# Performance work log

Measured on AMD Instinct MI355X. Metric: run time of the kernel, lower is better.

Reference implementation:

```python
import jax, jax.numpy as jnp
import numpy as np

D_MODEL = 2048
N_HEADS = 16
N_KV_HEADS = 4
HEAD_DIM = 128
ROPE_THETA = 1000000.0
B, T = 2, 2048


def setup_inputs() -> dict:
    key = jax.random.key(0)
    ks = jax.random.split(key, 5)
    s_in = 1.0 / np.sqrt(D_MODEL)
    s_o = 1.0 / np.sqrt(N_HEADS * HEAD_DIM)
    return {
        "x": jax.random.normal(ks[0], (B, T, D_MODEL), jnp.float32),
        "w_q": jax.random.normal(ks[1], (N_HEADS * HEAD_DIM, D_MODEL), jnp.float32) * s_in,
        "w_k": jax.random.normal(ks[2], (N_KV_HEADS * HEAD_DIM, D_MODEL), jnp.float32) * s_in,
        "w_v": jax.random.normal(ks[3], (N_KV_HEADS * HEAD_DIM, D_MODEL), jnp.float32) * s_in,
        "w_o": jax.random.normal(ks[4], (D_MODEL, N_HEADS * HEAD_DIM), jnp.float32) * s_o,
    }


def _rope_cos_sin(T, dtype):
    # inv_freq over even dims, emb = concat(freqs, freqs) (HF/llama convention)
    inv_freq = 1.0 / (ROPE_THETA ** (jnp.arange(0, HEAD_DIM, 2, dtype=jnp.float32) / HEAD_DIM))
    freqs = jnp.arange(T, dtype=jnp.float32)[:, None] * inv_freq[None, :]  # [T, hd/2]
    emb = jnp.concatenate([freqs, freqs], axis=-1)  # [T, hd]
    return jnp.cos(emb).astype(dtype), jnp.sin(emb).astype(dtype)


def _rotate_half(x):
    x1, x2 = jnp.split(x, 2, axis=-1)
    return jnp.concatenate([-x2, x1], axis=-1)


def reference(x, w_q, w_k, w_v, w_o):
    B, T, D = x.shape
    # QKV projections (bias=False), split heads -> [B, H, T, hd]
    q = (x @ w_q.T).reshape(B, T, N_HEADS, HEAD_DIM).transpose(0, 2, 1, 3)
    k = (x @ w_k.T).reshape(B, T, N_KV_HEADS, HEAD_DIM).transpose(0, 2, 1, 3)
    v = (x @ w_v.T).reshape(B, T, N_KV_HEADS, HEAD_DIM).transpose(0, 2, 1, 3)
    # RoPE
    cos, sin = _rope_cos_sin(T, x.dtype)  # [T, hd]
    q = q * cos + _rotate_half(q) * sin
    k = k * cos + _rotate_half(k) * sin
    # GQA: expand kv heads (repeat_interleave over head dim)
    rep = N_HEADS // N_KV_HEADS
    k = jnp.repeat(k, rep, axis=1)
    v = jnp.repeat(v, rep, axis=1)
    # Eager attention: QK^T * scale + causal mask, softmax, PV
    scale = HEAD_DIM ** -0.5
    scores = jnp.einsum("bhtd,bhsd->bhts", q, k) * scale
    causal = jnp.tril(jnp.ones((T, T), dtype=bool))
    scores = jnp.where(causal[None, None], scores, jnp.finfo(scores.dtype).min)
    probs = jax.nn.softmax(scores, axis=-1)
    out = jnp.einsum("bhts,bhsd->bhtd", probs, v)  # [B, H, T, hd]
    out = out.transpose(0, 2, 1, 3).reshape(B, T, N_HEADS * HEAD_DIM)
    return out @ w_o.T
```

## Files before the change

### kernel.cpp

```cpp
#include <hip/hip_runtime.h>
#include <cstdint>
#include <cstddef>

typedef unsigned short u16;
typedef unsigned u32;
typedef unsigned long long u64;
typedef __attribute__((ext_vector_type(8))) short short8;
typedef __attribute__((ext_vector_type(4))) float f32x4;

#define T_SEQ 2048
#define DM    2048
#define NHEAD 16
#define NKV   4
#define HD    128
#define NEGBIG (-3.0e38f)
#define QSCALE 0.1275525165017459f
#define L2IF (-0.31143258583318043f)

__device__ __forceinline__ u16 f2bf(float f) {
  union { float f; unsigned u; } c; c.f = f;
  return (u16)((c.u + 0x7fffu + ((c.u >> 16) & 1u)) >> 16);
}
__device__ __forceinline__ float bf2f(u16 b) {
  union { float f; unsigned u; } c; c.u = ((unsigned)b) << 16;
  return c.f;
}
__device__ __forceinline__ void gl_lds16(const u16* g, u16* l) {
  __builtin_amdgcn_global_load_lds(
      (const __attribute__((address_space(1))) void*)g,
      (__attribute__((address_space(3))) void*)l, 16, 0, 0);
}

#define FENCE() asm volatile("" ::: "memory")
#define BAR() do { FENCE(); __builtin_amdgcn_s_barrier(); FENCE(); } while (0)
#define WAITV4() asm volatile("s_waitcnt vmcnt(4)" ::: "memory")
#define WAITV3() asm volatile("s_waitcnt vmcnt(3)" ::: "memory")
#define WAITV0() asm volatile("s_waitcnt vmcnt(0)" ::: "memory")

__global__ void castk_all(const float* __restrict__ x, const float* __restrict__ wq,
                          const float* __restrict__ wk, const float* __restrict__ wv,
                          const float* __restrict__ wo, u16* __restrict__ dst) {
  long long i4 = (long long)blockIdx.x * 256 + threadIdx.x;
  const float* src; long long off;
  if (i4 < (2LL << 20))                    { src = x;  off = i4; }
  else if (i4 < (3LL << 20))               { src = wq; off = i4 - (2LL << 20); }
  else if (i4 < (3LL << 20) + (1 << 18))   { src = wk; off = i4 - (3LL << 20); }
  else if (i4 < (3LL << 20) + (2 << 18))   { src = wv; off = i4 - (3LL << 20) - (1 << 18); }
  else                                     { src = wo; off = i4 - (3LL << 20) - (2 << 18); }
  float4 v = *(const float4*)(src + off * 4);
  u16* d = dst + i4 * 4;
  d[0] = f2bf(v.x); d[1] = f2bf(v.y); d[2] = f2bf(v.z); d[3] = f2bf(v.w);
}

__global__ void tabk(float2* __restrict__ Tab) {
  int idx = blockIdx.x * 256 + threadIdx.x;
  float ang = (float)(idx >> 6) * exp2f((float)(idx & 63) * L2IF);
  float sn, cs;
  sincosf(ang, &sn, &cs);
  Tab[idx] = make_float2(cs, sn);
}

__global__ void ropek(u16* __restrict__ buf, const float2* __restrict__ Tab) {
  int idx = blockIdx.x * 256 + threadIdx.x;
  int r = idx >> 6, i = idx & 63;
  int t = r & (T_SEQ - 1);
  float2 cs = Tab[(t << 6) + i];
  size_t base = (size_t)r * HD + i;
  float x1 = bf2f(buf[base]), x2 = bf2f(buf[base + 64]);
  buf[base]      = f2bf(x1 * cs.x - x2 * cs.y);
  buf[base + 64] = f2bf(x2 * cs.x + x1 * cs.y);
}


template <int FH>
__device__ __forceinline__ void mfma_quad(f32x4 (&acc)[8][4], const short8 (&af)[4],
                                          const short8 (&bfr)[4]) {
#pragma unroll
  for (int i = 0; i < 4; ++i)
#pragma unroll
    for (int j = 0; j < 4; ++j)
      acc[FH * 4 + i][j] =
          __builtin_amdgcn_mfma_f32_16x16x32_bf16(af[i], bfr[j], acc[FH * 4 + i][j], 0, 0, 0);
}

template <int MODE>
__global__ __launch_bounds__(512, 2) void gemm8(
    const u16* __restrict__ A, const u16* __restrict__ Bm,
    void* __restrict__ Out0, u16* __restrict__ OutK, u16* __restrict__ OutV,
    int M, int N, int K) {
  __shared__ __align__(16) u16 AS[2][2][256 * 32];
  __shared__ __align__(16) u16 BS[2][2][256 * 32];
  const int tid = threadIdx.x;
  const int l = tid & 63, lm = l & 15, q = l >> 4;
  const int w = tid >> 6, wr = w >> 2, wc = w & 3;
  const int m0 = blockIdx.y * 256, n0 = blockIdx.x * 256;
  const u16* Ab = A + (size_t)m0 * K;
  const u16* Bb = Bm + (size_t)n0 * K;

  const int r0 = tid >> 2, r1 = 128 + (tid >> 2);
  const int sc = (((tid & 3) ^ ((tid >> 3) & 3))) * 8;
  const int rs = (lm >> 1) & 3;

#define STG_A(T, KC) do { \
    const int kb_ = (T) * 64 + (KC) * 32; \
    gl_lds16(Ab + (size_t)r0 * K + kb_ + sc, &AS[(T) & 1][KC][tid * 8]); \
    gl_lds16(Ab + (size_t)r1 * K + kb_ + sc, &AS[(T) & 1][KC][(512 + tid) * 8]); \
  } while (0)
#define STG_B(T, KC) do { \
    const int kb_ = (T) * 64 + (KC) * 32; \
    gl_lds16(Bb + (size_t)r0 * K + kb_ + sc, &BS[(T) & 1][KC][tid * 8]); \
    gl_lds16(Bb + (size_t)r1 * K + kb_ + sc, &BS[(T) & 1][KC][(512 + tid) * 8]); \
  } while (0)

  f32x4 acc[8][4] = {};
  const int nt = K >> 6;

  STG_A(0, 0); STG_B(0, 0);
  STG_A(0, 1); STG_B(0, 1);
  STG_A(1, 0); STG_B(1, 0);
  WAITV4();
  BAR();

  for (int t = 0; t < nt; ++t) {
    const int cur = t & 1;
    short8 bfr[4];

    {
      short8 af[4];
#pragma unroll
      for (int i = 0; i < 4; ++i)
        bfr[i] = *(const short8*)(&BS[cur][0][(wc * 64 + i * 16 + lm) * 32 + (q ^ rs) * 8]);
#pragma unroll
      for (int i = 0; i < 4; ++i)
        af[i] = *(const short8*)(&AS[cur][0][(wr * 128 + i * 16 + lm) * 32 + (q ^ rs) * 8]);
      if (t + 1 < nt) STG_A(t + 1, 1);
      BAR();
      __builtin_amdgcn_s_setprio(1);
      mfma_quad<0>(acc, af, bfr);
      __builtin_amdgcn_s_setprio(0);
      BAR();
    }
    {
      short8 af[4];
#pragma unroll
      for (int i = 0; i < 4; ++i)
        af[i] = *(const short8*)(&AS[cur][0][(wr * 128 + (4 + i) * 16 + lm) * 32 + (q ^ rs) * 8]);
      if (t + 1 < nt) STG_B(t + 1, 1);
      BAR();
      __builtin_amdgcn_s_setprio(1);
      mfma_quad<1>(acc, af, bfr);
      __builtin_amdgcn_s_setprio(0);
      BAR();
    }
    {
      short8 af[4];
#pragma unroll
      for (int i = 0; i < 4; ++i)
        bfr[i] = *(const short8*)(&BS[cur][1][(wc * 64 + i * 16 + lm) * 32 + (q ^ rs) * 8]);
#pragma unroll
      for (int i = 0; i < 4; ++i)
        af[i] = *(const short8*)(&AS[cur][1][(wr * 128 + i * 16 + lm) * 32 + (q ^ rs) * 8]);
      if (t + 2 < nt) STG_A(t + 2, 0);
      BAR();
      __builtin_amdgcn_s_setprio(1);
      mfma_quad<0>(acc, af, bfr);
      __builtin_amdgcn_s_setprio(0);
      BAR();
    }
    {
      short8 af[4];
#pragma unroll
      for (int i = 0; i < 4; ++i)
        af[i] = *(const short8*)(&AS[cur][1][(wr * 128 + (4 + i) * 16 + lm) * 32 + (q ^ rs) * 8]);
      if (t + 2 < nt) STG_B(t + 2, 0);
      BAR();
      __builtin_amdgcn_s_setprio(1);
      mfma_quad<1>(acc, af, bfr);
      __builtin_amdgcn_s_setprio(0);
      if (t < nt - 2) { WAITV4(); } else { WAITV0(); }
      BAR();
    }
  }
#undef STG_A
#undef STG_B

#pragma unroll
  for (int fm = 0; fm < 8; ++fm)
#pragma unroll
    for (int fn = 0; fn < 4; ++fn)
#pragma unroll
      for (int r = 0; r < 4; ++r) {
        int m = m0 + wr * 128 + fm * 16 + q * 4 + r;
        int n = n0 + wc * 64 + fn * 16 + lm;
        float v = acc[fm][fn][r];
        if constexpr (MODE == 0) {
          ((float*)Out0)[(size_t)m * N + n] = v;
        } else {
          int b = m >> 11, tt = m & (T_SEQ - 1);
          if (n < 2048) {
            int h = n >> 7, d = n & (HD - 1);
            ((u16*)Out0)[(((size_t)(b * NHEAD + h)) * T_SEQ + tt) * HD + d] = f2bf(v * QSCALE);
          } else if (n < 2560) {
            int nn = n - 2048, h = nn >> 7, d = nn & (HD - 1);
            OutK[(((size_t)(b * NKV + h)) * T_SEQ + tt) * HD + d] = f2bf(v);
          } else {
            int nn = n - 2560, h = nn >> 7, d = nn & (HD - 1);
            OutV[(((size_t)(b * NKV + h)) * HD + d) * T_SEQ + tt] = f2bf(v);
          }
        }
      }
}

__global__ __launch_bounds__(512, 2) void gemm8n(
    const u16* __restrict__ A, const u16* __restrict__ Bm,
    float* __restrict__ Out, int M, int N, int K) {
  __shared__ __align__(16) u16 AS[2][2][128 * 32];
  __shared__ __align__(16) u16 BS[2][2][256 * 32];
  const int tid = threadIdx.x;
  const int l = tid & 63, lm = l & 15, q = l >> 4;
  const int w = tid >> 6, wr = w >> 2, wc = w & 3;
  const int m0 = blockIdx.y * 128, n0 = blockIdx.x * 256;
  const u16* Ab = A + (size_t)m0 * K;
  const u16* Bb = Bm + (size_t)n0 * K;

  const int r0 = tid >> 2, r1 = 128 + (tid >> 2);
  const int sc = (((tid & 3) ^ ((tid >> 3) & 3))) * 8;
  const int rs = (lm >> 1) & 3;

#define STG_A(T, KC) \
    gl_lds16(Ab + (size_t)r0 * K + (T) * 64 + (KC) * 32 + sc, &AS[(T) & 1][KC][tid * 8])
#define STG_B(T, KC) do { \
    const int kb_ = (T) * 64 + (KC) * 32; \
    gl_lds16(Bb + (size_t)r0 * K + kb_ + sc, &BS[(T) & 1][KC][tid * 8]); \
    gl_lds16(Bb + (size_t)r1 * K + kb_ + sc, &BS[(T) & 1][KC][(512 + tid) * 8]); \
  } while (0)

  f32x4 acc[4][4] = {};
  const int nt = K >> 6;

  STG_A(0, 0); STG_B(0, 0);
  STG_A(0, 1); STG_B(0, 1);
  STG_A(1, 0); STG_B(1, 0);
  WAITV3();
  BAR();

  for (int t = 0; t < nt; ++t) {
    const int cur = t & 1;
    {
      short8 af[4], bfr[4];
#pragma unroll
      for (int i = 0; i < 4; ++i)
        bfr[i] = *(const short8*)(&BS[cur][0][(wc * 64 + i * 16 + lm) * 32 + (q ^ rs) * 8]);
#pragma unroll
      for (int i = 0; i < 4; ++i)
        af[i] = *(const short8*)(&AS[cur][0][(wr * 64 + i * 16 + lm) * 32 + (q ^ rs) * 8]);
      if (t + 1 < nt) { STG_A(t + 1, 1); STG_B(t + 1, 1); }
      BAR();
      __builtin_amdgcn_s_setprio(1);
#pragma unroll
      for (int i = 0; i < 4; ++i)
#pragma unroll
        for (int j = 0; j < 4; ++j)
          acc[i][j] = __builtin_amdgcn_mfma_f32_16x16x32_bf16(af[i], bfr[j], acc[i][j], 0, 0, 0);
      __builtin_amdgcn_s_setprio(0);
      BAR();
    }
    {
      short8 af[4], bfr[4];
#pragma unroll
      for (int i = 0; i < 4; ++i)
        bfr[i] = *(const short8*)(&BS[cur][1][(wc * 64 + i * 16 + lm) * 32 + (q ^ rs) * 8]);
#pragma unroll
      for (int i = 0; i < 4; ++i)
        af[i] = *(const short8*)(&AS[cur][1][(wr * 64 + i * 16 + lm) * 32 + (q ^ rs) * 8]);
      if (t + 2 < nt) { STG_A(t + 2, 0); STG_B(t + 2, 0); }
      BAR();
      __builtin_amdgcn_s_setprio(1);
#pragma unroll
      for (int i = 0; i < 4; ++i)
#pragma unroll
        for (int j = 0; j < 4; ++j)
          acc[i][j] = __builtin_amdgcn_mfma_f32_16x16x32_bf16(af[i], bfr[j], acc[i][j], 0, 0, 0);
      __builtin_amdgcn_s_setprio(0);
      if (t < nt - 2) { WAITV3(); } else { WAITV0(); }
      BAR();
    }
  }
#undef STG_A
#undef STG_B

#pragma unroll
  for (int fm = 0; fm < 4; ++fm)
#pragma unroll
    for (int fn = 0; fn < 4; ++fn)
#pragma unroll
      for (int r = 0; r < 4; ++r) {
        int m = m0 + wr * 64 + fm * 16 + q * 4 + r;
        int n = n0 + wc * 64 + fn * 16 + lm;
        Out[(size_t)m * N + n] = acc[fm][fn][r];
      }
}

#define PSTRIDE 72
__global__ __launch_bounds__(256, 2) void attnk(
    const u16* __restrict__ Q, const u16* __restrict__ Kh,
    const u16* __restrict__ Vt, const float2* __restrict__ Tab,
    u16* __restrict__ Oa) {
  __shared__ __align__(16) u16 Ks[2][64 * 128];
  __shared__ __align__(16) u16 Vs[2][128 * 64];
  __shared__ __align__(16) u16 Pl[4][16 * PSTRIDE];
  const int tid = threadIdx.x;
  const int w = tid >> 6, l = tid & 63, lm = l & 15, q = l >> 4;

  const int wg = blockIdx.x;
  const int g = wg & 7, slot = wg >> 3;
  const int b = g >> 2, kvh = g & 3;
  const int h = kvh * 4 + (slot & 3);
  const int p = slot >> 2;

  const u16* Kb = Kh + ((size_t)(b * NKV + kvh)) * T_SEQ * HD;
  const u16* Vb = Vt + ((size_t)(b * NKV + kvh)) * HD * T_SEQ;
  u16* Pw = Pl[w];

  const int r16 = tid >> 4, c16 = tid & 15;
  const int r8  = tid >> 3, c8  = tid & 7;

#pragma unroll 1
  for (int half = 0; half < 2; ++half) {
    const int tile = half ? p : (31 - p);
    const int tbase = tile * 64 + w * 16;
    const u16* Qb = Q + (((size_t)(b * NHEAD + h)) * T_SEQ + tbase) * HD;

    short8 qa[4];
#pragma unroll
    for (int ks = 0; ks < 4; ++ks)
      qa[ks] = *(const short8*)(Qb + (size_t)lm * HD + ks * 32 + q * 8);

    {
      const float2* tb = Tab + (((size_t)(tbase + lm)) << 6) + q * 8;
#pragma unroll
      for (int ks = 0; ks < 2; ++ks) {
        short8 lo = qa[ks], hi = qa[ks + 2];
#pragma unroll
        for (int e = 0; e < 8; ++e) {
          float2 cs = tb[ks * 32 + e];
          float x1 = bf2f((u16)lo[e]), x2 = bf2f((u16)hi[e]);
          lo[e] = (short)f2bf(x1 * cs.x - x2 * cs.y);
          hi[e] = (short)f2bf(x2 * cs.x + x1 * cs.y);
        }
        qa[ks] = lo; qa[ks + 2] = hi;
      }
    }

    float m_i = NEGBIG, l_i = 0.f;
    f32x4 oacc[8] = {};
    const int nst = tile + 1;

    {
#pragma unroll
      for (int j = 0; j < 4; ++j) {
        int s = j * 16 + r16, gs = c16 ^ (s & 15);
        gl_lds16(Kb + (size_t)s * HD + gs * 8, &Ks[0][s * 128 + c16 * 8]);
      }
#pragma unroll
      for (int j = 0; j < 4; ++j) {
        int d = j * 32 + r8, gs = c8 ^ (d & 7);
        gl_lds16(Vb + (size_t)d * T_SEQ + gs * 8, &Vs[0][d * 64 + c8 * 8]);
      }
    }
    __syncthreads();

    for (int st = 0; st < nst; ++st) {
      const int bb = st & 1;
      if (st + 1 < nst) {
        const int s0n = (st + 1) * 64;
#pragma unroll
        for (int j = 0; j < 4; ++j) {
          int s = j * 16 + r16, gs = c16 ^ (s & 15);
          gl_lds16(Kb + (size_t)(s0n + s) * HD + gs * 8, &Ks[bb ^ 1][s * 128 + c16 * 8]);
        }
#pragma unroll
        for (int j = 0; j < 4; ++j) {
          int d = j * 32 + r8, gs = c8 ^ (d & 7);
          gl_lds16(Vb + (size_t)d * T_SEQ + s0n + gs * 8, &Vs[bb ^ 1][d * 64 + c8 * 8]);
        }
      }

      f32x4 sacc[4] = {};
#pragma unroll
      for (int ks = 0; ks < 4; ++ks)
#pragma unroll
        for (int nt = 0; nt < 4; ++nt) {
          short8 kb = *(const short8*)(&Ks[bb][(nt * 16 + lm) * 128 + ((ks * 4 + q) ^ lm) * 8]);
          sacc[nt] = __builtin_amdgcn_mfma_f32_16x16x32_bf16(kb, qa[ks], sacc[nt], 0, 0, 0);
        }

      const bool diag = (st == nst - 1);
      const int s0 = st * 64;
      float mx = NEGBIG;
#pragma unroll
      for (int nt = 0; nt < 4; ++nt)
#pragma unroll
        for (int j = 0; j < 4; ++j) {
          float v = sacc[nt][j];
          if (diag) {
            int s_abs = s0 + nt * 16 + q * 4 + j;
            if (s_abs > tbase + lm) v = NEGBIG;
            sacc[nt][j] = v;
          }
          mx = fmaxf(mx, v);
        }
      mx = fmaxf(mx, __shfl_xor(mx, 16, 64));
      mx = fmaxf(mx, __shfl_xor(mx, 32, 64));
      if (__any(mx > m_i + 8.0f)) {
        float mnew = fmaxf(m_i, mx);
        float alpha = exp2f(m_i - mnew);
        m_i = mnew;
        l_i *= alpha;
#pragma unroll
        for (int dt = 0; dt < 8; ++dt)
#pragma unroll
          for (int j = 0; j < 4; ++j) oacc[dt][j] *= alpha;
      }
      float sum = 0.f;
#pragma unroll
      for (int nt = 0; nt < 4; ++nt) {
        float e0 = exp2f(sacc[nt][0] - m_i), e1 = exp2f(sacc[nt][1] - m_i);
        float e2 = exp2f(sacc[nt][2] - m_i), e3 = exp2f(sacc[nt][3] - m_i);
        sum += (e0 + e1) + (e2 + e3);
        u32 lo32 = __builtin_amdgcn_perm(__float_as_uint(e1), __float_as_uint(e0), 0x07060302u);
        u32 hi32 = __builtin_amdgcn_perm(__float_as_uint(e3), __float_as_uint(e2), 0x07060302u);
        *(u64*)(Pw + lm * PSTRIDE + nt * 16 + q * 4) = ((u64)hi32 << 32) | lo32;
      }
      sum += __shfl_xor(sum, 16, 64);
      sum += __shfl_xor(sum, 32, 64);
      l_i += sum;

      asm volatile("" ::: "memory");

#pragma unroll
      for (int ks = 0; ks < 2; ++ks) {
        short8 pa = *(const short8*)(Pw + lm * PSTRIDE + ks * 32 + q * 8);
#pragma unroll
        for (int dt = 0; dt < 8; ++dt) {
          short8 vb = *(const short8*)(
              &Vs[bb][(dt * 16 + lm) * 64 + ((ks * 4 + q) ^ (lm & 7)) * 8]);
          oacc[dt] = __builtin_amdgcn_mfma_f32_16x16x32_bf16(vb, pa, oacc[dt], 0, 0, 0);
        }
      }
      __syncthreads();
    }

    float inv = 1.0f / l_i;
    int t = tbase + lm;
#pragma unroll
    for (int dt = 0; dt < 8; ++dt) {
      u16 ok[4];
#pragma unroll
      for (int j = 0; j < 4; ++j) ok[j] = f2bf(oacc[dt][j] * inv);
      *(u64*)(Oa + ((size_t)(b * T_SEQ + t)) * (NHEAD * HD) + h * HD + dt * 16 + q * 4) =
          (u64)ok[0] | ((u64)ok[1] << 16) | ((u64)ok[2] << 32) | ((u64)ok[3] << 48);
    }
  }
}

extern "C" void kernel_launch(void* const* d_in, const int* in_sizes, int n_in,
                              void* d_out, int out_size, void* d_ws, size_t ws_size,
                              hipStream_t stream) {
  const float* x  = (const float*)d_in[0];
  const float* wq = (const float*)d_in[1];
  const float* wk = (const float*)d_in[2];
  const float* wv = (const float*)d_in[3];
  const float* wo = (const float*)d_in[4];
  float* out = (float*)d_out;

  u16* ws  = (u16*)d_ws;
  u16* xb  = ws;
  u16* wqb = xb  + (8u << 20);
  u16* wkb = wqb + (4u << 20);
  u16* wvb = wkb + (1u << 20);
  u16* wob = wvb + (1u << 20);
  u16* Qb  = wob + (4u << 20);
  u16* Kb  = Qb  + (8u << 20);
  u16* Vtb = Kb  + (2u << 20);
  u16* Ab  = xb;
  float2* tab = (float2*)wkb;

  castk_all<<<18432, 256, 0, stream>>>(x, wq, wk, wv, wo, ws);

  gemm8<3><<<dim3(12, 16), 512, 0, stream>>>(xb, wqb, Qb, Kb, Vtb, 4096, 3072, 2048);

  tabk<<<512, 256, 0, stream>>>(tab);
  ropek<<<4096, 256, 0, stream>>>(Kb, tab);

  attnk<<<512, 256, 0, stream>>>(Qb, Kb, Vtb, tab, Ab);

  gemm8n<<<dim3(8, 32), 512, 0, stream>>>(Ab, wob, out, 4096, 2048, 2048);
}
```

Baseline: 316.4 us.

## Restructure GEMM LDS tiles to 64-wide rows with XOR swizzle and XCD-aware block remap

Both projection GEMMs now stage each 64-wide K slice as one row-major LDS tile with an 8-way XOR swizzle, replacing the two 32-wide sub-tiles. The global-to-LDS load schedule is reordered and the vmcnt waits are adjusted to match. Blocks are launched on a 1D grid and remapped so that consecutive tiles land on the same XCD, which is meant to improve L2 reuse. The output GEMM also splits each half-step into two N-halves to spread loads across more barrier phases. The cost is extra barriers per iteration and a runtime MODE check in place of the template parameter.

```diff
diff --git a/kernel.cpp b/kernel.cpp
--- a/kernel.cpp
+++ b/kernel.cpp
@@ -33,8 +33,7 @@
 
 #define FENCE() asm volatile("" ::: "memory")
 #define BAR() do { FENCE(); __builtin_amdgcn_s_barrier(); FENCE(); } while (0)
-#define WAITV4() asm volatile("s_waitcnt vmcnt(4)" ::: "memory")
-#define WAITV3() asm volatile("s_waitcnt vmcnt(3)" ::: "memory")
+#define WAITV2() asm volatile("s_waitcnt vmcnt(2)" ::: "memory")
 #define WAITV0() asm volatile("s_waitcnt vmcnt(0)" ::: "memory")
 
 __global__ void castk_all(const float* __restrict__ x, const float* __restrict__ wq,
@@ -83,42 +82,39 @@
           __builtin_amdgcn_mfma_f32_16x16x32_bf16(af[i], bfr[j], acc[FH * 4 + i][j], 0, 0, 0);
 }
 
-template <int MODE>
 __global__ __launch_bounds__(512, 2) void gemm8(
     const u16* __restrict__ A, const u16* __restrict__ Bm,
     void* __restrict__ Out0, u16* __restrict__ OutK, u16* __restrict__ OutV,
     int M, int N, int K) {
-  __shared__ __align__(16) u16 AS[2][2][256 * 32];
-  __shared__ __align__(16) u16 BS[2][2][256 * 32];
+  __shared__ __align__(16) u16 AS[2][256 * 64];
+  __shared__ __align__(16) u16 BS[2][256 * 64];
   const int tid = threadIdx.x;
   const int l = tid & 63, lm = l & 15, q = l >> 4;
   const int w = tid >> 6, wr = w >> 2, wc = w & 3;
-  const int m0 = blockIdx.y * 256, n0 = blockIdx.x * 256;
+  const int nid = (blockIdx.x & 7) * 24 + (blockIdx.x >> 3);
+  const int by = nid / 12, bx = nid - by * 12;
+  const int m0 = by * 256, n0 = bx * 256;
   const u16* Ab = A + (size_t)m0 * K;
   const u16* Bb = Bm + (size_t)n0 * K;
 
-  const int r0 = tid >> 2, r1 = 128 + (tid >> 2);
-  const int sc = (((tid & 3) ^ ((tid >> 3) & 3))) * 8;
-  const int rs = (lm >> 1) & 3;
-
-#define STG_A(T, KC) do { \
-    const int kb_ = (T) * 64 + (KC) * 32; \
-    gl_lds16(Ab + (size_t)r0 * K + kb_ + sc, &AS[(T) & 1][KC][tid * 8]); \
-    gl_lds16(Ab + (size_t)r1 * K + kb_ + sc, &AS[(T) & 1][KC][(512 + tid) * 8]); \
-  } while (0)
-#define STG_B(T, KC) do { \
-    const int kb_ = (T) * 64 + (KC) * 32; \
-    gl_lds16(Bb + (size_t)r0 * K + kb_ + sc, &BS[(T) & 1][KC][tid * 8]); \
-    gl_lds16(Bb + (size_t)r1 * K + kb_ + sc, &BS[(T) & 1][KC][(512 + tid) * 8]); \
-  } while (0)
+  const int srow = tid >> 3;
+  const int scol = ((tid & 7) ^ (srow & 7)) * 8;
+  const int rsw = lm & 7;
+
+#define STG_A(T, U) \
+  gl_lds16(Ab + (size_t)((U) * 64 + srow) * K + (T) * 64 + scol, \
+           &AS[(T) & 1][((U) * 512 + tid) * 8])
+#define STG_B(T, U) \
+  gl_lds16(Bb + (size_t)((U) * 64 + srow) * K + (T) * 64 + scol, \
+           &BS[(T) & 1][((U) * 512 + tid) * 8])
 
   f32x4 acc[8][4] = {};
   const int nt = K >> 6;
 
-  STG_A(0, 0); STG_B(0, 0);
-  STG_A(0, 1); STG_B(0, 1);
-  STG_A(1, 0); STG_B(1, 0);
-  WAITV4();
+  STG_A(0, 0); STG_A(0, 2); STG_A(0, 1); STG_A(0, 3);
+  STG_B(0, 0); STG_B(0, 1); STG_B(0, 2); STG_B(0, 3);
+  STG_A(1, 0); STG_A(1, 2);
+  WAITV2();
   BAR();
 
   for (int t = 0; t < nt; ++t) {
@@ -129,11 +125,11 @@
       short8 af[4];
 #pragma unroll
       for (int i = 0; i < 4; ++i)
-        bfr[i] = *(const short8*)(&BS[cur][0][(wc * 64 + i * 16 + lm) * 32 + (q ^ rs) * 8]);
-#pragma unroll
-      for (int i = 0; i < 4; ++i)
-        af[i] = *(const short8*)(&AS[cur][0][(wr * 128 + i * 16 + lm) * 32 + (q ^ rs) * 8]);
-      if (t + 1 < nt) STG_A(t + 1, 1);
+        bfr[i] = *(const short8*)(&BS[cur][(wc * 64 + i * 16 + lm) * 64 + (q ^ rsw) * 8]);
+#pragma unroll
+      for (int i = 0; i < 4; ++i)
+        af[i] = *(const short8*)(&AS[cur][(wr * 128 + i * 16 + lm) * 64 + (q ^ rsw) * 8]);
+      if (t + 1 < nt) { STG_A(t + 1, 1); STG_A(t + 1, 3); }
       BAR();
       __builtin_amdgcn_s_setprio(1);
       mfma_quad<0>(acc, af, bfr);
@@ -144,8 +140,8 @@
       short8 af[4];
 #pragma unroll
       for (int i = 0; i < 4; ++i)
-        af[i] = *(const short8*)(&AS[cur][0][(wr * 128 + (4 + i) * 16 + lm) * 32 + (q ^ rs) * 8]);
-      if (t + 1 < nt) STG_B(t + 1, 1);
+        af[i] = *(const short8*)(&AS[cur][(wr * 128 + (4 + i) * 16 + lm) * 64 + (q ^ rsw) * 8]);
+      if (t + 1 < nt) { STG_B(t + 1, 0); STG_B(t + 1, 1); }
       BAR();
       __builtin_amdgcn_s_setprio(1);
       mfma_quad<1>(acc, af, bfr);
@@ -156,11 +152,11 @@
       short8 af[4];
 #pragma unroll
       for (int i = 0; i < 4; ++i)
-        bfr[i] = *(const short8*)(&BS[cur][1][(wc * 64 + i * 16 + lm) * 32 + (q ^ rs) * 8]);
-#pragma unroll
-      for (int i = 0; i < 4; ++i)
-        af[i] = *(const short8*)(&AS[cur][1][(wr * 128 + i * 16 + lm) * 32 + (q ^ rs) * 8]);
-      if (t + 2 < nt) STG_A(t + 2, 0);
+        bfr[i] = *(const short8*)(&BS[cur][(wc * 64 + i * 16 + lm) * 64 + ((4 + q) ^ rsw) * 8]);
+#pragma unroll
+      for (int i = 0; i < 4; ++i)
+        af[i] = *(const short8*)(&AS[cur][(wr * 128 + i * 16 + lm) * 64 + ((4 + q) ^ rsw) * 8]);
+      if (t + 1 < nt) { STG_B(t + 1, 2); STG_B(t + 1, 3); }
       BAR();
       __builtin_amdgcn_s_setprio(1);
       mfma_quad<0>(acc, af, bfr);
@@ -171,19 +167,20 @@
       short8 af[4];
 #pragma unroll
       for (int i = 0; i < 4; ++i)
-        af[i] = *(const short8*)(&AS[cur][1][(wr * 128 + (4 + i) * 16 + lm) * 32 + (q ^ rs) * 8]);
-      if (t + 2 < nt) STG_B(t + 2, 0);
+        af[i] = *(const short8*)(&AS[cur][(wr * 128 + (4 + i) * 16 + lm) * 64 + ((4 + q) ^ rsw) * 8]);
+      if (t + 2 < nt) { STG_A(t + 2, 0); STG_A(t + 2, 2); }
       BAR();
       __builtin_amdgcn_s_setprio(1);
       mfma_quad<1>(acc, af, bfr);
       __builtin_amdgcn_s_setprio(0);
-      if (t < nt - 2) { WAITV4(); } else { WAITV0(); }
+      if (t < nt - 2) { WAITV2(); } else { WAITV0(); }
       BAR();
     }
   }
 #undef STG_A
 #undef STG_B
 
+  const int MODE = (N == 3072) ? 3 : 0;
 #pragma unroll
   for (int fm = 0; fm < 8; ++fm)
 #pragma unroll
@@ -193,7 +190,7 @@
         int m = m0 + wr * 128 + fm * 16 + q * 4 + r;
         int n = n0 + wc * 64 + fn * 16 + lm;
         float v = acc[fm][fn][r];
-        if constexpr (MODE == 0) {
+        if (MODE == 0) {
           ((float*)Out0)[(size_t)m * N + n] = v;
         } else {
           int b = m >> 11, tt = m & (T_SEQ - 1);
@@ -214,75 +211,109 @@
 __global__ __launch_bounds__(512, 2) void gemm8n(
     const u16* __restrict__ A, const u16* __restrict__ Bm,
     float* __restrict__ Out, int M, int N, int K) {
-  __shared__ __align__(16) u16 AS[2][2][128 * 32];
-  __shared__ __align__(16) u16 BS[2][2][256 * 32];
+  __shared__ __align__(16) u16 AS[2][128 * 64];
+  __shared__ __align__(16) u16 BS[2][256 * 64];
   const int tid = threadIdx.x;
   const int l = tid & 63, lm = l & 15, q = l >> 4;
   const int w = tid >> 6, wr = w >> 2, wc = w & 3;
-  const int m0 = blockIdx.y * 128, n0 = blockIdx.x * 256;
+  const int nid = (blockIdx.x & 7) * 32 + (blockIdx.x >> 3);
+  const int by = nid >> 3, bx = nid & 7;
+  const int m0 = by * 128, n0 = bx * 256;
   const u16* Ab = A + (size_t)m0 * K;
   const u16* Bb = Bm + (size_t)n0 * K;
 
-  const int r0 = tid >> 2, r1 = 128 + (tid >> 2);
-  const int sc = (((tid & 3) ^ ((tid >> 3) & 3))) * 8;
-  const int rs = (lm >> 1) & 3;
-
-#define STG_A(T, KC) \
-    gl_lds16(Ab + (size_t)r0 * K + (T) * 64 + (KC) * 32 + sc, &AS[(T) & 1][KC][tid * 8])
-#define STG_B(T, KC) do { \
-    const int kb_ = (T) * 64 + (KC) * 32; \
-    gl_lds16(Bb + (size_t)r0 * K + kb_ + sc, &BS[(T) & 1][KC][tid * 8]); \
-    gl_lds16(Bb + (size_t)r1 * K + kb_ + sc, &BS[(T) & 1][KC][(512 + tid) * 8]); \
-  } while (0)
+  const int srow = tid >> 3;
+  const int scol = ((tid & 7) ^ (srow & 7)) * 8;
+  const int rsw = lm & 7;
+
+#define STG_A(T, U) \
+  gl_lds16(Ab + (size_t)((U) * 64 + srow) * K + (T) * 64 + scol, \
+           &AS[(T) & 1][((U) * 512 + tid) * 8])
+#define STG_B(T, U) \
+  gl_lds16(Bb + (size_t)((U) * 64 + srow) * K + (T) * 64 + scol, \
+           &BS[(T) & 1][((U) * 512 + tid) * 8])
 
   f32x4 acc[4][4] = {};
   const int nt = K >> 6;
 
-  STG_A(0, 0); STG_B(0, 0);
-  STG_A(0, 1); STG_B(0, 1);
-  STG_A(1, 0); STG_B(1, 0);
-  WAITV3();
+  STG_A(0, 0); STG_A(0, 1);
+  STG_B(0, 0); STG_B(0, 1); STG_B(0, 2); STG_B(0, 3);
+  STG_A(1, 0); STG_A(1, 1);
+  WAITV2();
   BAR();
 
   for (int t = 0; t < nt; ++t) {
     const int cur = t & 1;
-    {
-      short8 af[4], bfr[4];
-#pragma unroll
-      for (int i = 0; i < 4; ++i)
-        bfr[i] = *(const short8*)(&BS[cur][0][(wc * 64 + i * 16 + lm) * 32 + (q ^ rs) * 8]);
-#pragma unroll
-      for (int i = 0; i < 4; ++i)
-        af[i] = *(const short8*)(&AS[cur][0][(wr * 64 + i * 16 + lm) * 32 + (q ^ rs) * 8]);
-      if (t + 1 < nt) { STG_A(t + 1, 1); STG_B(t + 1, 1); }
-      BAR();
-      __builtin_amdgcn_s_setprio(1);
-#pragma unroll
-      for (int i = 0; i < 4; ++i)
-#pragma unroll
-        for (int j = 0; j < 4; ++j)
+    short8 af[4];
+
+    {
+      short8 bfr[2];
+#pragma unroll
+      for (int j = 0; j < 2; ++j)
+        bfr[j] = *(const short8*)(&BS[cur][(wc * 64 + j * 16 + lm) * 64 + (q ^ rsw) * 8]);
+#pragma unroll
+      for (int i = 0; i < 4; ++i)
+        af[i] = *(const short8*)(&AS[cur][(wr * 64 + i * 16 + lm) * 64 + (q ^ rsw) * 8]);
+      if (t + 1 < nt) { STG_B(t + 1, 0); STG_B(t + 1, 1); }
+      BAR();
+      __builtin_amdgcn_s_setprio(1);
+#pragma unroll
+      for (int i = 0; i < 4; ++i)
+#pragma unroll
+        for (int j = 0; j < 2; ++j)
           acc[i][j] = __builtin_amdgcn_mfma_f32_16x16x32_bf16(af[i], bfr[j], acc[i][j], 0, 0, 0);
       __builtin_amdgcn_s_setprio(0);
       BAR();
     }
     {
-      short8 af[4], bfr[4];
-#pragma unroll
-      for (int i = 0; i < 4; ++i)
-        bfr[i] = *(const short8*)(&BS[cur][1][(wc * 64 + i * 16 + lm) * 32 + (q ^ rs) * 8]);
-#pragma unroll
-      for (int i = 0; i < 4; ++i)
-        af[i] = *(const short8*)(&AS[cur][1][(wr * 64 + i * 16 + lm) * 32 + (q ^ rs) * 8]);
-      if (t + 2 < nt) { STG_A(t + 2, 0); STG_B(t + 2, 0); }
-      BAR();
-      __builtin_amdgcn_s_setprio(1);
-#pragma unroll
-      for (int i = 0; i < 4; ++i)
-#pragma unroll
-        for (int j = 0; j < 4; ++j)
+      short8 bfr[2];
+#pragma unroll
+      for (int j = 0; j < 2; ++j)
+        bfr[j] = *(const short8*)(&BS[cur][(wc * 64 + (2 + j) * 16 + lm) * 64 + (q ^ rsw) * 8]);
+      if (t + 1 < nt) { STG_B(t + 1, 2); STG_B(t + 1, 3); }
+      BAR();
+      __builtin_amdgcn_s_setprio(1);
+#pragma unroll
+      for (int i = 0; i < 4; ++i)
+#pragma unroll
+        for (int j = 0; j < 2; ++j)
+          acc[i][2 + j] = __builtin_amdgcn_mfma_f32_16x16x32_bf16(af[i], bfr[j], acc[i][2 + j], 0, 0, 0);
+      __builtin_amdgcn_s_setprio(0);
+      BAR();
+    }
+    {
+      short8 bfr[2];
+#pragma unroll
+      for (int j = 0; j < 2; ++j)
+        bfr[j] = *(const short8*)(&BS[cur][(wc * 64 + j * 16 + lm) * 64 + ((4 + q) ^ rsw) * 8]);
+#pragma unroll
+      for (int i = 0; i < 4; ++i)
+        af[i] = *(const short8*)(&AS[cur][(wr * 64 + i * 16 + lm) * 64 + ((4 + q) ^ rsw) * 8]);
+      BAR();
+      __builtin_amdgcn_s_setprio(1);
+#pragma unroll
+      for (int i = 0; i < 4; ++i)
+#pragma unroll
+        for (int j = 0; j < 2; ++j)
           acc[i][j] = __builtin_amdgcn_mfma_f32_16x16x32_bf16(af[i], bfr[j], acc[i][j], 0, 0, 0);
       __builtin_amdgcn_s_setprio(0);
-      if (t < nt - 2) { WAITV3(); } else { WAITV0(); }
+      BAR();
+    }
+    {
+      short8 bfr[2];
+#pragma unroll
+      for (int j = 0; j < 2; ++j)
+        bfr[j] = *(const short8*)(&BS[cur][(wc * 64 + (2 + j) * 16 + lm) * 64 + ((4 + q) ^ rsw) * 8]);
+      if (t + 2 < nt) { STG_A(t + 2, 0); STG_A(t + 2, 1); }
+      BAR();
+      __builtin_amdgcn_s_setprio(1);
+#pragma unroll
+      for (int i = 0; i < 4; ++i)
+#pragma unroll
+        for (int j = 0; j < 2; ++j)
+          acc[i][2 + j] = __builtin_amdgcn_mfma_f32_16x16x32_bf16(af[i], bfr[j], acc[i][2 + j], 0, 0, 0);
+      __builtin_amdgcn_s_setprio(0);
+      if (t < nt - 2) { WAITV2(); } else { WAITV0(); }
       BAR();
     }
   }
@@ -488,12 +519,12 @@
 
   castk_all<<<18432, 256, 0, stream>>>(x, wq, wk, wv, wo, ws);
 
-  gemm8<3><<<dim3(12, 16), 512, 0, stream>>>(xb, wqb, Qb, Kb, Vtb, 4096, 3072, 2048);
+  gemm8<<<192, 512, 0, stream>>>(xb, wqb, Qb, Kb, Vtb, 4096, 3072, 2048);
 
   tabk<<<512, 256, 0, stream>>>(tab);
   ropek<<<4096, 256, 0, stream>>>(Kb, tab);
 
   attnk<<<512, 256, 0, stream>>>(Qb, Kb, Vtb, tab, Ab);
 
-  gemm8n<<<dim3(8, 32), 512, 0, stream>>>(Ab, wob, out, 4096, 2048, 2048);
-}
+  gemm8n<<<256, 512, 0, stream>>>(Ab, wob, out, 4096, 2048, 2048);
+}
```

New measurement: 318.7 us. No clear change (+0.7%).
